# Optimization experiments

Hardware: AMD Instinct MI355X
Metric: run time of the kernel (lower is better)

## Reference

```python
import jax, jax.numpy as jnp
import numpy as np

B, IMG_LEN, TXT_LEN = 32, 49, 77
D, H, HK, FF, NB = 512, 8, 64, 2048, 4
IMG_DIM, VOCAB = 768, 49408
L = IMG_LEN + TXT_LEN

# combined mask: image tokens attend fully; text tokens causal among themselves
_row = np.arange(L)
_KEEP = jnp.asarray(~((_row[:, None] >= IMG_LEN) & (_row[None, :] >= IMG_LEN) & (_row[None, :] > _row[:, None])))  # [L,L] bool


def setup_inputs():
    key = jax.random.key(0)
    ks = jax.random.split(key, 12)
    s = 0.02
    z = lambda *sh: jnp.zeros(sh, jnp.float32)
    o = lambda *sh: jnp.ones(sh, jnp.float32)
    n = lambda k, sh: jax.random.normal(k, sh, jnp.float32) * s
    return {
        'img_hidden': jax.random.normal(ks[0], (B, IMG_LEN, IMG_DIM), jnp.float32),
        'txt_embed': jax.random.normal(ks[1], (B, TXT_LEN, D), jnp.float32),
        'img_proj_w': n(ks[2], (IMG_DIM, D)), 'img_proj_b': z(D),
        'pos_embed': n(ks[3], (L, D)),
        'wq': n(ks[4], (NB, H, D, HK)), 'wk': n(ks[5], (NB, H, D, HK)), 'wv': n(ks[6], (NB, H, D, HK)),
        'w_proj': n(ks[7], (NB, D, D)), 'b_proj': z(NB, D),
        'ln1_g': o(NB, D), 'ln1_b': z(NB, D), 'ln2_g': o(NB, D), 'ln2_b': z(NB, D),
        'fc1_w': n(ks[8], (NB, D, FF)), 'fc1_b': z(NB, FF),
        'fc2_w': n(ks[9], (NB, FF, D)), 'fc2_b': z(NB, D),
        'lnf_g': o(D), 'lnf_b': z(D),
        'out_w': n(ks[10], (D, VOCAB)), 'out_b': z(VOCAB),
        'attention_mask': jnp.ones((B, TXT_LEN), jnp.int32),
    }


def _ln(x, g, b, eps=1e-5):
    mu = x.mean(-1, keepdims=True)
    var = ((x - mu) ** 2).mean(-1, keepdims=True)
    return (x - mu) * jax.lax.rsqrt(var + eps) * g + b


def _forward(img_hidden, txt_embed, img_proj_w, img_proj_b, pos_embed, wq, wk, wv, w_proj, b_proj,
             ln1_g, ln1_b, ln2_g, ln2_b, fc1_w, fc1_b, fc2_w, fc2_b, lnf_g, lnf_b, out_w, out_b,
             attention_mask):
    img = img_hidden @ img_proj_w + img_proj_b + pos_embed[:IMG_LEN]
    txt = txt_embed + pos_embed[IMG_LEN:]
    x = jnp.concatenate([img, txt], axis=1)  # [B,L,D]
    pad = jnp.concatenate([jnp.ones((x.shape[0], IMG_LEN), attention_mask.dtype), attention_mask], axis=1)
    keep = _KEEP[None, None] & (pad[:, None, None, :] != 0)  # [B,1,L,L]
    scale = D ** (-0.5)  # NOTE: original scales by full embed_dim, not head_size (faithful)
    for i in range(NB):
        h = _ln(x, ln1_g[i], ln1_b[i])
        q = jnp.einsum('bld,hdk->bhlk', h, wq[i])
        k = jnp.einsum('bld,hdk->bhlk', h, wk[i])
        v = jnp.einsum('bld,hdk->bhlk', h, wv[i])
        scores = jnp.einsum('bhlk,bhmk->bhlm', q, k) * scale
        scores = jnp.where(keep, scores, -jnp.inf)
        aw = jax.nn.softmax(scores, axis=-1)  # dropout off (eval)
        o = jnp.einsum('bhlm,bhmk->bhlk', aw, v)
        o = o.transpose(0, 2, 1, 3).reshape(x.shape[0], L, H * HK)
        x = x + o @ w_proj[i] + b_proj[i]
        h2 = _ln(x, ln2_g[i], ln2_b[i])
        x = x + jax.nn.gelu(h2 @ fc1_w[i] + fc1_b[i], approximate=False) @ fc2_w[i] + fc2_b[i]
    x = _ln(x, lnf_g, lnf_b)
    return x[:, IMG_LEN:] @ out_w + out_b  # [B,TXT_LEN,VOCAB]


def reference(img_hidden, txt_embed, img_proj_w, img_proj_b, pos_embed, wq, wk, wv, w_proj, b_proj,
              ln1_g, ln1_b, ln2_g, ln2_b, fc1_w, fc1_b, fc2_w, fc2_b, lnf_g, lnf_b, out_w, out_b,
              attention_mask):
    return _forward(img_hidden, txt_embed, img_proj_w, img_proj_b, pos_embed, wq, wk, wv, w_proj, b_proj,
                    ln1_g, ln1_b, ln2_g, ln2_b, fc1_w, fc1_b, fc2_w, fc2_b, lnf_g, lnf_b, out_w, out_b,
                    attention_mask)
```

## Files before the change

### kernel.cpp

```cpp
#include <hip/hip_runtime.h>
#include <hip/hip_bf16.h>
#include <stdint.h>


using u16 = unsigned short;
typedef __attribute__((ext_vector_type(8))) __bf16 bf16x8v;
typedef __attribute__((ext_vector_type(4))) float f32x4;

__device__ __forceinline__ float bf2f(u16 u) {
  union { unsigned int i; float f; } x; x.i = ((unsigned int)u) << 16; return x.f;
}
__device__ __forceinline__ u16 f2bf(float f) {
  union { float f; unsigned int i; } u; u.f = f;
  unsigned int r = u.i + 0x7FFFu + ((u.i >> 16) & 1u);
  return (u16)(r >> 16);
}
__device__ __forceinline__ float ld_f(const void* p, size_t i, int fl) {
  return fl ? ((const float*)p)[i] : bf2f(((const u16*)p)[i]);
}
__device__ __forceinline__ u16 ld_bf(const void* p, size_t i, int fl) {
  return fl ? f2bf(((const float*)p)[i]) : ((const u16*)p)[i];
}

__device__ __forceinline__ void async_copy16(const void* g, void* l) {
  __builtin_amdgcn_global_load_lds(
      (__attribute__((address_space(1))) void*)(g),
      (__attribute__((address_space(3))) void*)(l), 16, 0, 0);
}

__global__ void detect_kernel(const void* __restrict__ img, int* __restrict__ flag) {
  const int lane = threadIdx.x;
  const u16* p = (const u16*)img;
  int bad = 0;
#pragma unroll
  for (int i = 0; i < 4; ++i) {
    float v = bf2f(p[lane * 4 + i]);
    float av = fabsf(v);
    if (!(av <= 1e4f) || (av != 0.0f && av < 1e-30f)) bad++;
  }
#pragma unroll
  for (int off = 32; off; off >>= 1) bad += __shfl_xor(bad, off, 64);
  if (lane == 0) flag[0] = (bad > 16) ? 1 : 0;
}

__global__ void sentinel_kernel(float* out) {
  out[blockIdx.x * 256 + threadIdx.x] = 123456.0f;
}

template <int BM, int BN, int EPI>
__global__ __launch_bounds__(256) void gemm_kernel(
    const u16* __restrict__ A, const u16* __restrict__ Bt, void* Cout,
    const void* __restrict__ bias, long boff, const float* resid,
    const void* __restrict__ pos, int M, int N, int K, int gridM,
    const int* __restrict__ fl)
{
  static_assert(BN == 128, "");
  static_assert(BM == 64 || BM == 128, "");
  constexpr int TILE_B = (BM + BN) * 128;
  constexpr int EPI_B = BM * BN * 2;
  constexpr int SMEM_B = (2 * TILE_B > EPI_B) ? 2 * TILE_B : EPI_B;
  __shared__ __align__(16) char smem[SMEM_B];

  const int tid = threadIdx.x;
  const int lane = tid & 63, wid = tid >> 6;
  const int wm = wid >> 1, wn = wid & 1;
  constexpr int FM = BM / 32, FN = 4;
  constexpr int ITA = BM / 32, ITB = BN / 32;
  constexpr int NLOADS = ITA + ITB;

  const int nwg = gridDim.x;
  const int q = nwg >> 3, r8 = nwg & 7;
  const int xcd = blockIdx.x & 7, idx = blockIdx.x >> 3;
  const int wgid = (xcd < r8 ? xcd * (q + 1) : r8 * (q + 1) + (xcd - r8) * q) + idx;
  const int tileM = (wgid % gridM) * BM, tileN = (wgid / gridM) * BN;

  f32x4 acc[FM][FN] = {};

  auto stage = [&](int buf, int kt) {
    char* base = smem + buf * TILE_B;
#pragma unroll
    for (int it = 0; it < ITA; ++it) {
      int ch = (wid * ITA + it) * 64 + lane;
      int row = ch >> 3, slot = ch & 7;
      int grow = tileM + row; grow = grow < M ? grow : (M - 1);
      async_copy16(A + (size_t)grow * K + kt * 64 + ((slot ^ (row & 7)) << 3),
                   base + (wid * ITA + it) * 1024);
    }
#pragma unroll
    for (int it = 0; it < ITB; ++it) {
      int ch = (wid * ITB + it) * 64 + lane;
      int row = ch >> 3, slot = ch & 7;
      async_copy16(Bt + (size_t)(tileN + row) * K + kt * 64 + ((slot ^ (row & 7)) << 3),
                   base + BM * 128 + (wid * ITB + it) * 1024);
    }
  };

  const int kSteps = K >> 6;
  stage(0, 0);
  int cur = 0;
  for (int kt = 0; kt < kSteps; ++kt) {
    if (kt + 1 < kSteps) {
      stage(cur ^ 1, kt + 1);
      asm volatile("s_waitcnt vmcnt(%0)" :: "i"(NLOADS) : "memory");
    } else {
      asm volatile("s_waitcnt vmcnt(0)" ::: "memory");
    }
    __builtin_amdgcn_s_barrier();
    __builtin_amdgcn_sched_barrier(0);
    const u16* lA = (const u16*)(smem + cur * TILE_B);
    const u16* lB = (const u16*)(smem + cur * TILE_B + BM * 128);
#pragma unroll
    for (int kk = 0; kk < 2; ++kk) {
      const int j = kk * 4 + (lane >> 4);
      bf16x8v af[FM], bfr[FN];
#pragma unroll
      for (int fm = 0; fm < FM; ++fm) {
        int rr = wm * (BM / 2) + fm * 16 + (lane & 15);
        af[fm] = *(const bf16x8v*)(lA + rr * 64 + ((j ^ (rr & 7)) << 3));
      }
#pragma unroll
      for (int fn = 0; fn < FN; ++fn) {
        int rn = wn * 64 + fn * 16 + (lane & 15);
        bfr[fn] = *(const bf16x8v*)(lB + rn * 64 + ((j ^ (rn & 7)) << 3));
      }
      __builtin_amdgcn_s_setprio(1);
#pragma unroll
      for (int fm = 0; fm < FM; ++fm)
#pragma unroll
        for (int fn = 0; fn < FN; ++fn)
          acc[fm][fn] = __builtin_amdgcn_mfma_f32_16x16x32_bf16(
              af[fm], bfr[fn], acc[fm][fn], 0, 0, 0);
      __builtin_amdgcn_s_setprio(0);
    }
    __builtin_amdgcn_sched_barrier(0);
    __builtin_amdgcn_s_barrier();
    cur ^= 1;
  }

  const int fla = (EPI == 0) ? 0 : *fl;
  const int row0l = wm * (BM / 2);
  const int col0l = wn * 64;

  auto store_bf16 = [&](bool do_bias, bool do_gelu) {
    u16* ep = (u16*)smem;
#pragma unroll
    for (int fm = 0; fm < FM; ++fm)
#pragma unroll
      for (int fn = 0; fn < FN; ++fn)
#pragma unroll
        for (int jj = 0; jj < 4; ++jj) {
          int rl = row0l + fm * 16 + ((lane >> 4) << 2) + jj;
          int cl = col0l + fn * 16 + (lane & 15);
          float t = acc[fm][fn][jj];
          if (do_bias) t += ld_f(bias, boff + tileN + cl, fla);
          if (do_gelu) t = 0.5f * t * (1.0f + erff(t * 0.70710678118654752f));
          ep[rl * BN + cl] = f2bf(t);
        }
    __syncthreads();
    for (int rr = tid >> 4; rr < BM; rr += 16) {
      int grow = tileM + rr;
      if (grow < M)
        *(uint4*)((u16*)Cout + (size_t)grow * N + tileN + (tid & 15) * 8) =
            *(const uint4*)(ep + rr * BN + (tid & 15) * 8);
    }
  };

  auto store_f32 = [&](bool do_resid, bool do_remap_pos) {
    float* epf = (float*)smem;
#pragma unroll
    for (int p = 0; p < 2; ++p) {
      __syncthreads();
      if (wm == p) {
#pragma unroll
        for (int fm = 0; fm < FM; ++fm)
#pragma unroll
          for (int fn = 0; fn < FN; ++fn)
#pragma unroll
            for (int jj = 0; jj < 4; ++jj) {
              int rl = fm * 16 + ((lane >> 4) << 2) + jj;
              int cl = col0l + fn * 16 + (lane & 15);
              float t = acc[fm][fn][jj] + ld_f(bias, boff + tileN + cl, fla);
              if (do_remap_pos) {
                int grow_t = tileM + p * (BM / 2) + rl;
                int ll = grow_t % 49;
                t += ld_f(pos, ll * 512 + tileN + cl, fla);
              }
              epf[rl * BN + cl] = t;
            }
      }
      __syncthreads();
      for (int rr = tid >> 5; rr < BM / 2; rr += 8) {
        int grow = tileM + p * (BM / 2) + rr;
        if (grow < M) {
          f32x4 t = *(const f32x4*)(epf + rr * BN + (tid & 31) * 4);
          if (do_resid)
            t += *(const f32x4*)(resid + (size_t)grow * N + tileN + (tid & 31) * 4);
          size_t orow = grow;
          if (do_remap_pos) orow = (size_t)(grow / 49) * 126 + grow % 49;
          *(f32x4*)((float*)Cout + orow * N + tileN + (tid & 31) * 4) = t;
        }
      }
    }
  };

  if constexpr (EPI == 0) store_bf16(false, false);
  else if constexpr (EPI == 1) store_bf16(true, true);
  else if constexpr (EPI == 2) store_f32(true, false);
  else if constexpr (EPI == 3) store_f32(false, true);
  else { if (fla) store_f32(false, false); else store_bf16(true, false); }
}

__global__ __launch_bounds__(512) void gemm256_kernel(
    const u16* __restrict__ A, const u16* __restrict__ Bt, void* Cout,
    const void* __restrict__ bias, int M, int N, int K, int gridM,
    const int* __restrict__ fl)
{
  constexpr int BM = 256, BN = 256;
  constexpr int TILE_B = (BM + BN) * 128;
  __shared__ __align__(16) char smem[2 * TILE_B];

  const int tid = threadIdx.x;
  const int lane = tid & 63, wid = tid >> 6;
  const int wm = wid >> 2, wn = wid & 3;

  const int nwg = gridDim.x;
  const int q = nwg >> 3, r8 = nwg & 7;
  const int xcd = blockIdx.x & 7, idx = blockIdx.x >> 3;
  const int wgid = (xcd < r8 ? xcd * (q + 1) : r8 * (q + 1) + (xcd - r8) * q) + idx;
  const int tileM = (wgid % gridM) * BM, tileN = (wgid / gridM) * BN;

  f32x4 acc[8][4] = {};

  auto stage = [&](int buf, int kt) {
    char* base = smem + buf * TILE_B;
#pragma unroll
    for (int it = 0; it < 4; ++it) {
      int ch = (wid * 4 + it) * 64 + lane;
      int row = ch >> 3, slot = ch & 7;
      int grow = tileM + row; grow = grow < M ? grow : (M - 1);
      async_copy16(A + (size_t)grow * K + kt * 64 + ((slot ^ (row & 7)) << 3),
                   base + (wid * 4 + it) * 1024);
    }
#pragma unroll
    for (int it = 0; it < 4; ++it) {
      int ch = (wid * 4 + it) * 64 + lane;
      int row = ch >> 3, slot = ch & 7;
      async_copy16(Bt + (size_t)(tileN + row) * K + kt * 64 + ((slot ^ (row & 7)) << 3),
                   base + BM * 128 + (wid * 4 + it) * 1024);
    }
  };

  const int kSteps = K >> 6;
  stage(0, 0);
  int cur = 0;
  for (int kt = 0; kt < kSteps; ++kt) {
    if (kt + 1 < kSteps) {
      stage(cur ^ 1, kt + 1);
      asm volatile("s_waitcnt vmcnt(8)" ::: "memory");
    } else {
      asm volatile("s_waitcnt vmcnt(0)" ::: "memory");
    }
    __builtin_amdgcn_s_barrier();
    __builtin_amdgcn_sched_barrier(0);
    const u16* lA = (const u16*)(smem + cur * TILE_B);
    const u16* lB = (const u16*)(smem + cur * TILE_B + BM * 128);
#pragma unroll
    for (int kk = 0; kk < 2; ++kk) {
      const int j = kk * 4 + (lane >> 4);
      bf16x8v bfr[4];
#pragma unroll
      for (int fn = 0; fn < 4; ++fn) {
        int rn = wn * 64 + fn * 16 + (lane & 15);
        bfr[fn] = *(const bf16x8v*)(lB + rn * 64 + ((j ^ (rn & 7)) << 3));
      }
#pragma unroll
      for (int mh = 0; mh < 2; ++mh) {
        bf16x8v af[4];
#pragma unroll
        for (int f = 0; f < 4; ++f) {
          int rr = wm * 128 + (mh * 4 + f) * 16 + (lane & 15);
          af[f] = *(const bf16x8v*)(lA + rr * 64 + ((j ^ (rr & 7)) << 3));
        }
        __builtin_amdgcn_s_setprio(1);
#pragma unroll
        for (int f = 0; f < 4; ++f)
#pragma unroll
          for (int fn = 0; fn < 4; ++fn)
            acc[mh * 4 + f][fn] = __builtin_amdgcn_mfma_f32_16x16x32_bf16(
                af[f], bfr[fn], acc[mh * 4 + f][fn], 0, 0, 0);
        __builtin_amdgcn_s_setprio(0);
      }
    }
    __builtin_amdgcn_sched_barrier(0);
    __builtin_amdgcn_s_barrier();
    cur ^= 1;
  }

  const int fla = *fl;
  if (fla) {
    float* epf = (float*)smem;
#pragma unroll
    for (int p = 0; p < 4; ++p) {
      __syncthreads();
      if (wm == (p >> 1)) {
#pragma unroll
        for (int fq = 0; fq < 4; ++fq) {
          int fm = (p & 1) * 4 + fq;
#pragma unroll
          for (int fn = 0; fn < 4; ++fn)
#pragma unroll
            for (int jj = 0; jj < 4; ++jj) {
              int rl = fq * 16 + ((lane >> 4) << 2) + jj;
              int cl = wn * 64 + fn * 16 + (lane & 15);
              epf[rl * 256 + cl] = acc[fm][fn][jj] + ld_f(bias, tileN + cl, 1);
            }
        }
      }
      __syncthreads();
      for (int rr = tid >> 6; rr < 64; rr += 8) {
        int grow = tileM + p * 64 + rr;
        if (grow < M)
          *(f32x4*)((float*)Cout + (size_t)grow * N + tileN + lane * 4) =
              *(const f32x4*)(epf + rr * 256 + lane * 4);
      }
    }
  } else {
    u16* ep = (u16*)smem;
    __syncthreads();
#pragma unroll
    for (int fm = 0; fm < 8; ++fm)
#pragma unroll
      for (int fn = 0; fn < 4; ++fn)
#pragma unroll
        for (int jj = 0; jj < 4; ++jj) {
          int rl = wm * 128 + fm * 16 + ((lane >> 4) << 2) + jj;
          int cl = wn * 64 + fn * 16 + (lane & 15);
          ep[rl * 256 + cl] = f2bf(acc[fm][fn][jj] + ld_f(bias, tileN + cl, 0));
        }
    __syncthreads();
    for (int rr = tid >> 5; rr < 256; rr += 16) {
      int grow = tileM + rr;
      if (grow < M)
        *(uint4*)((u16*)Cout + (size_t)grow * N + tileN + (tid & 31) * 8) =
            *(const uint4*)(ep + rr * 256 + (tid & 31) * 8);
    }
  }
}

__global__ __launch_bounds__(256) void prep_all(
    const void* __restrict__ imgw, const void* __restrict__ wq,
    const void* __restrict__ wk, const void* __restrict__ wv,
    const void* __restrict__ wp, const void* __restrict__ fc1,
    const void* __restrict__ fc2, const void* __restrict__ imgh,
    const void* __restrict__ txt, const void* __restrict__ pos,
    u16* __restrict__ imgwT, u16* __restrict__ qkvT, u16* __restrict__ wpT,
    u16* __restrict__ fc1T, u16* __restrict__ fc2T,
    u16* __restrict__ imgbf, float* __restrict__ x,
    const int* __restrict__ fl)
{
  const int fla = *fl;
  const int b = blockIdx.x;
  if (b >= 12672) {
    if (b < 17376) {
      int i = (b - 12672) * 256 + threadIdx.x;
      if (i < 1204224) imgbf[i] = ld_bf(imgh, i, fla);
    } else {
      int idx = (b - 17376) * 256 + threadIdx.x;
      if (idx < 32 * 77 * 512) {
        int d = idx & 511, bt = idx >> 9;
        int t = bt % 77, bb = bt / 77;
        x[((size_t)(bb * 126 + 49 + t)) * 512 + d] =
            ld_f(txt, idx, fla) + ld_f(pos, (49 + t) * 512 + d, fla);
      }
    }
    return;
  }
  __shared__ u16 t[32][33];
  const void* in; u16* out; int R, C, cx, ry;
  size_t zi, zo;
  if (b < 384) {
    in = imgw; out = imgwT; R = 768; C = 512; zi = 0; zo = 0;
    cx = b & 15; ry = b >> 4;
  } else if (b < 3456) {
    int bb = b - 384;
    int z = bb >> 5, r2 = bb & 31;
    cx = r2 & 1; ry = r2 >> 1;
    int src = z >> 5, rem = z & 31, li = rem >> 3, hh = rem & 7;
    in = (src == 0) ? wq : (src == 1) ? wk : wv;
    out = qkvT; R = 512; C = 64;
    zi = (size_t)rem * (512 * 64);
    zo = (size_t)li * (1536 * 512) + (size_t)(src * 512 + hh * 64) * 512;
  } else if (b < 4480) {
    int bb = b - 3456;
    int z = bb >> 8, r2 = bb & 255;
    cx = r2 & 15; ry = r2 >> 4;
    in = wp; out = wpT; R = 512; C = 512;
    zi = (size_t)z * (512 * 512); zo = zi;
  } else if (b < 8576) {
    int bb = b - 4480;
    int z = bb >> 10, r2 = bb & 1023;
    cx = r2 & 63; ry = r2 >> 6;
    in = fc1; out = fc1T; R = 512; C = 2048;
    zi = (size_t)z * (512 * 2048); zo = zi;
  } else {
    int bb = b - 8576;
    int z = bb >> 10, r2 = bb & 1023;
    cx = r2 & 15; ry = r2 >> 4;
    in = fc2; out = fc2T; R = 2048; C = 512;
    zi = (size_t)z * (512 * 2048); zo = zi;
  }
  const int c0 = cx * 32, r0 = ry * 32;
  const int tx = threadIdx.x & 31, ty = threadIdx.x >> 5;
#pragma unroll
  for (int i = 0; i < 4; ++i)
    t[ty + 8 * i][tx] = ld_bf(in, zi + (size_t)(r0 + ty + 8 * i) * C + (c0 + tx), fla);
  __syncthreads();
#pragma unroll
  for (int i = 0; i < 4; ++i)
    out[zo + (size_t)(c0 + ty + 8 * i) * R + (r0 + tx)] = t[tx][ty + 8 * i];
}

__global__ __launch_bounds__(256) void transpose_lnf(
    const void* __restrict__ out_w, u16* __restrict__ outwT,
    const float* __restrict__ x, const void* __restrict__ gam,
    const void* __restrict__ bet, u16* __restrict__ xl,
    const int* __restrict__ fl)
{
  const int fla = *fl;
  const int b = blockIdx.x;
  if (b >= 24704) {
    const int lane = threadIdx.x & 63, wid = threadIdx.x >> 6;
    const int r = (b - 24704) * 4 + wid;
    if (r >= 2464) return;
    int bb = r / 77, t = r % 77;
    int srow = bb * 126 + 49 + t;
    const float* xr = x + (size_t)srow * 512 + lane * 8;
    f32x4 v0 = *(const f32x4*)xr;
    f32x4 v1 = *(const f32x4*)(xr + 4);
    float s = v0[0] + v0[1] + v0[2] + v0[3] + v1[0] + v1[1] + v1[2] + v1[3];
#pragma unroll
    for (int off = 32; off; off >>= 1) s += __shfl_xor(s, off, 64);
    const float mu = s * (1.0f / 512.0f);
    float q2 = 0.f;
#pragma unroll
    for (int j = 0; j < 4; ++j) { v0[j] -= mu; q2 += v0[j] * v0[j]; }
#pragma unroll
    for (int j = 0; j < 4; ++j) { v1[j] -= mu; q2 += v1[j] * v1[j]; }
#pragma unroll
    for (int off = 32; off; off >>= 1) q2 += __shfl_xor(q2, off, 64);
    const float inv = rsqrtf(q2 * (1.0f / 512.0f) + 1e-5f);
    union { u16 a[8]; uint4 v; } ou;
#pragma unroll
    for (int j = 0; j < 8; ++j) {
      float d = (j < 4) ? v0[j] : v1[j - 4];
      ou.a[j] = f2bf(d * inv * ld_f(gam, lane * 8 + j, fla)
                     + ld_f(bet, lane * 8 + j, fla));
    }
    *(uint4*)(xl + (size_t)r * 512 + lane * 8) = ou.v;
    return;
  }
  __shared__ u16 t[32][33];
  const int cx = b % 1544, ry = b / 1544;
  const int c0 = cx * 32, r0 = ry * 32;
  const int tx = threadIdx.x & 31, ty = threadIdx.x >> 5;
#pragma unroll
  for (int i = 0; i < 4; ++i)
    t[ty + 8 * i][tx] =
        ld_bf(out_w, (size_t)(r0 + ty + 8 * i) * 49408 + (c0 + tx), fla);
  __syncthreads();
#pragma unroll
  for (int i = 0; i < 4; ++i)
    outwT[(size_t)(c0 + ty + 8 * i) * 512 + (r0 + tx)] = t[tx][ty + 8 * i];
}

__global__ __launch_bounds__(256) void attn_mfma_kernel(
    const u16* __restrict__ qkv, const int* __restrict__ amask,
    u16* __restrict__ o)
{
  const int b = blockIdx.x, hh = blockIdx.y;
  __shared__ __align__(16) u16 Qs[128 * 64];
  __shared__ __align__(16) u16 Ks[128 * 64];
  __shared__ __align__(16) u16 Vt[64 * 136];
  __shared__ float Sf[128 * 129];
  __shared__ __align__(16) u16 Ps[128 * 128];
  __shared__ float padK[128];
  const int tid = threadIdx.x, lane = tid & 63, wid = tid >> 6;

  for (int ch = tid; ch < 1024; ch += 256) {
    int row = ch >> 3, slot = ch & 7;
    int gm = row < 126 ? row : 125;
    size_t base = ((size_t)(b * 126 + gm)) * 1536 + hh * 64;
    int gslot = slot ^ (row & 7);
    *(uint4*)(Qs + row * 64 + slot * 8) = *(const uint4*)(qkv + base + gslot * 8);
    *(uint4*)(Ks + row * 64 + slot * 8) = *(const uint4*)(qkv + base + 512 + gslot * 8);
  }
  for (int m = wid; m < 126; m += 4) {
    size_t base = ((size_t)(b * 126 + m)) * 1536 + hh * 64 + 1024;
    Vt[lane * 136 + m] = qkv[base + lane];
  }
  if (wid == 0) { Vt[lane * 136 + 126] = 0; Vt[lane * 136 + 127] = 0; }
  for (int j = tid; j < 128; j += 256) {
    float kv = 0.0f;
    if (j < 49) kv = 1.0f;
    else if (j < 126) kv = (amask[b * 77 + (j - 49)] != 0) ? 1.0f : 0.0f;
    padK[j] = kv;
  }
  __syncthreads();

  f32x4 accS[2][8] = {};
#pragma unroll
  for (int ks = 0; ks < 2; ++ks) {
    const int j = ks * 4 + (lane >> 4);
    bf16x8v qf[2], kf[8];
#pragma unroll
    for (int fr = 0; fr < 2; ++fr) {
      int rr = (wid * 2 + fr) * 16 + (lane & 15);
      qf[fr] = *(const bf16x8v*)(Qs + rr * 64 + ((j ^ (rr & 7)) << 3));
    }
#pragma unroll
    for (int fc = 0; fc < 8; ++fc) {
      int rn = fc * 16 + (lane & 15);
      kf[fc] = *(const bf16x8v*)(Ks + rn * 64 + ((j ^ (rn & 7)) << 3));
    }
#pragma unroll
    for (int fr = 0; fr < 2; ++fr)
#pragma unroll
      for (int fc = 0; fc < 8; ++fc)
        accS[fr][fc] = __builtin_amdgcn_mfma_f32_16x16x32_bf16(
            qf[fr], kf[fc], accS[fr][fc], 0, 0, 0);
  }
#pragma unroll
  for (int fr = 0; fr < 2; ++fr)
#pragma unroll
    for (int fc = 0; fc < 8; ++fc)
#pragma unroll
      for (int jj = 0; jj < 4; ++jj) {
        int row = (wid * 2 + fr) * 16 + ((lane >> 4) << 2) + jj;
        int col = fc * 16 + (lane & 15);
        Sf[row * 129 + col] = accS[fr][fc][jj];
      }
  __syncthreads();

  const float scale = 0.04419417382415922f;
  for (int r = wid; r < 128; r += 4) {
    const int m0 = lane, m1 = lane + 64;
    float s0 = Sf[r * 129 + m0] * scale;
    float s1 = Sf[r * 129 + m1] * scale;
    bool kp0 = (padK[m0] != 0.f) && (m0 < 49 || r < 49 || m0 <= r);
    bool kp1 = (padK[m1] != 0.f) && (r < 49 || m1 <= r);
    float e0 = kp0 ? s0 : -1e30f;
    float e1 = kp1 ? s1 : -1e30f;
    float mx = fmaxf(e0, e1);
#pragma unroll
    for (int off = 32; off; off >>= 1) mx = fmaxf(mx, __shfl_xor(mx, off, 64));
    float p0 = kp0 ? __expf(s0 - mx) : 0.f;
    float p1 = kp1 ? __expf(s1 - mx) : 0.f;
    float sm = p0 + p1;
#pragma unroll
    for (int off = 32; off; off >>= 1) sm += __shfl_xor(sm, off, 64);
    float inv = 1.0f / sm;
    Ps[r * 128 + (((m0 >> 3) ^ (r & 7)) << 3) + (m0 & 7)] = f2bf(p0 * inv);
    Ps[r * 128 + (((m1 >> 3) ^ (r & 7)) << 3) + (m1 & 7)] = f2bf(p1 * inv);
  }
  __syncthreads();

  f32x4 accO[2][4] = {};
#pragma unroll
  for (int ks = 0; ks < 4; ++ks) {
    const int j = ks * 4 + (lane >> 4);
    bf16x8v pf[2], vf[4];
#pragma unroll
    for (int fr = 0; fr < 2; ++fr) {
      int rr = (wid * 2 + fr) * 16 + (lane & 15);
      pf[fr] = *(const bf16x8v*)(Ps + rr * 128 + ((j ^ (rr & 7)) << 3));
    }
#pragma unroll
    for (int fc = 0; fc < 4; ++fc) {
      int rn = fc * 16 + (lane & 15);
      vf[fc] = *(const bf16x8v*)(Vt + rn * 136 + (j << 3));
    }
#pragma unroll
    for (int fr = 0; fr < 2; ++fr)
#pragma unroll
      for (int fc = 0; fc < 4; ++fc)
        accO[fr][fc] = __builtin_amdgcn_mfma_f32_16x16x32_bf16(
            pf[fr], vf[fc], accO[fr][fc], 0, 0, 0);
  }

  u16* Ol = Qs;
  __syncthreads();
#pragma unroll
  for (int fr = 0; fr < 2; ++fr)
#pragma unroll
    for (int fc = 0; fc < 4; ++fc)
#pragma unroll
      for (int jj = 0; jj < 4; ++jj) {
        int row = (wid * 2 + fr) * 16 + ((lane >> 4) << 2) + jj;
        int col = fc * 16 + (lane & 15);
        Ol[row * 64 + col] = f2bf(accO[fr][fc][jj]);
      }
  __syncthreads();
  for (int r = tid >> 3; r < 126; r += 32) {
    *(uint4*)(o + ((size_t)(b * 126 + r)) * 512 + hh * 64 + (tid & 7) * 8) =
        *(const uint4*)(Ol + r * 64 + (tid & 7) * 8);
  }
}

__global__ __launch_bounds__(256) void ln_kernel(
    const float* __restrict__ x, const void* __restrict__ gam,
    const void* __restrict__ bet, long goff, u16* __restrict__ out,
    int nrows, const int* __restrict__ fl)
{
  const int fla = *fl;
  const int lane = threadIdx.x & 63, wid = threadIdx.x >> 6;
  const int r = blockIdx.x * 4 + wid;
  if (r >= nrows) return;
  const float* xr = x + (size_t)r * 512 + lane * 8;
  f32x4 v0 = *(const f32x4*)xr;
  f32x4 v1 = *(const f32x4*)(xr + 4);
  float s = v0[0] + v0[1] + v0[2] + v0[3] + v1[0] + v1[1] + v1[2] + v1[3];
#pragma unroll
  for (int off = 32; off; off >>= 1) s += __shfl_xor(s, off, 64);
  const float mu = s * (1.0f / 512.0f);
  float q2 = 0.f;
#pragma unroll
  for (int j = 0; j < 4; ++j) { v0[j] -= mu; q2 += v0[j] * v0[j]; }
#pragma unroll
  for (int j = 0; j < 4; ++j) { v1[j] -= mu; q2 += v1[j] * v1[j]; }
#pragma unroll
  for (int off = 32; off; off >>= 1) q2 += __shfl_xor(q2, off, 64);
  const float inv = rsqrtf(q2 * (1.0f / 512.0f) + 1e-5f);
  union { u16 a[8]; uint4 v; } ou;
#pragma unroll
  for (int j = 0; j < 8; ++j) {
    float d = (j < 4) ? v0[j] : v1[j - 4];
    ou.a[j] = f2bf(d * inv * ld_f(gam, goff + lane * 8 + j, fla)
                   + ld_f(bet, goff + lane * 8 + j, fla));
  }
  *(uint4*)(out + (size_t)r * 512 + lane * 8) = ou.v;
}

extern "C" void kernel_launch(void* const* d_in, const int* in_sizes, int n_in,
                              void* d_out, int out_size, void* d_ws, size_t ws_size,
                              hipStream_t stream)
{
  (void)in_sizes; (void)n_in; (void)out_size;
  const void* img_hidden = d_in[0];
  const void* txt_emb    = d_in[1];
  const void* img_proj_w = d_in[2];
  const void* img_proj_b = d_in[3];
  const void* pos_embed  = d_in[4];
  const void* wq    = d_in[5];
  const void* wk    = d_in[6];
  const void* wv    = d_in[7];
  const void* w_proj = d_in[8];
  const void* b_proj = d_in[9];
  const void* ln1_g = d_in[10];
  const void* ln1_b = d_in[11];
  const void* ln2_g = d_in[12];
  const void* ln2_b = d_in[13];
  const void* fc1_w = d_in[14];
  const void* fc1_b = d_in[15];
  const void* fc2_w = d_in[16];
  const void* fc2_b = d_in[17];
  const void* lnf_g = d_in[18];
  const void* lnf_b = d_in[19];
  const void* out_w = d_in[20];
  const void* out_b = d_in[21];
  const int* amask  = (const int*)d_in[22];

  char* ws = (char*)d_ws;
  size_t off = 0;
  auto alloc = [&](size_t bytes) {
    void* p = ws + off; off += (bytes + 255) & ~(size_t)255; return p;
  };
  int* dflag = (int*)alloc(256);
  u16* imgbf = (u16*)alloc(1204224ull * 2);
  float* x   = (float*)alloc(4032ull * 512 * 4);
  u16* xl    = (u16*)alloc(2464ull * 512 * 2);
  const size_t uni0 = off;
  u16* imgwT = (u16*)alloc(512ull * 768 * 2);
  u16* qkvT  = (u16*)alloc(4ull * 1536 * 512 * 2);
  u16* wpT   = (u16*)alloc(4ull * 512 * 512 * 2);
  u16* fc1T  = (u16*)alloc(4ull * 2048 * 512 * 2);
  u16* fc2T  = (u16*)alloc(4ull * 512 * 2048 * 2);
  u16* h     = (u16*)alloc(4032ull * 512 * 2);
  u16* qkvb  = (u16*)alloc(4032ull * 1536 * 2);
  u16* ob    = (u16*)alloc(4032ull * 512 * 2);
  u16* ff    = (u16*)alloc(4032ull * 2048 * 2);
  u16* outwT = (u16*)(ws + uni0);

  if (ws_size < off) {
    sentinel_kernel<<<dim3(16), 256, 0, stream>>>((float*)d_out);
    return;
  }

  detect_kernel<<<dim3(1), 64, 0, stream>>>(img_hidden, dflag);
  prep_all<<<dim3(22304), 256, 0, stream>>>(
      img_proj_w, wq, wk, wv, w_proj, fc1_w, fc2_w, img_hidden, txt_emb,
      pos_embed, imgwT, qkvT, wpT, fc1T, fc2T, imgbf, x, dflag);

  gemm_kernel<64, 128, 3><<<dim3(100), 256, 0, stream>>>(
      imgbf, imgwT, x, img_proj_b, 0, nullptr, pos_embed, 1568, 512, 768, 25, dflag);

  for (int i = 0; i < 4; ++i) {
    ln_kernel<<<dim3(1008), 256, 0, stream>>>(x, ln1_g, ln1_b, i * 512, h, 4032, dflag);
    gemm_kernel<64, 128, 0><<<dim3(756), 256, 0, stream>>>(
        h, qkvT + i * 786432, qkvb, nullptr, 0, nullptr, nullptr, 4032, 1536, 512, 63, dflag);
    attn_mfma_kernel<<<dim3(32, 8), 256, 0, stream>>>(qkvb, amask, ob);
    gemm_kernel<64, 128, 2><<<dim3(252), 256, 0, stream>>>(
        ob, wpT + i * 262144, x, b_proj, i * 512, x, nullptr, 4032, 512, 512, 63, dflag);
    ln_kernel<<<dim3(1008), 256, 0, stream>>>(x, ln2_g, ln2_b, i * 512, h, 4032, dflag);
    gemm_kernel<64, 128, 1><<<dim3(1008), 256, 0, stream>>>(
        h, fc1T + i * 1048576, ff, fc1_b, i * 2048, nullptr, nullptr, 4032, 2048, 512, 63, dflag);
    gemm_kernel<64, 128, 2><<<dim3(252), 256, 0, stream>>>(
        ff, fc2T + i * 1048576, x, fc2_b, i * 512, x, nullptr, 4032, 512, 2048, 63, dflag);
  }

  transpose_lnf<<<dim3(25320), 256, 0, stream>>>(
      out_w, outwT, x, lnf_g, lnf_b, xl, dflag);
  gemm256_kernel<<<dim3(1930), 512, 0, stream>>>(
      xl, outwT, d_out, out_b, 2464, 49408, 512, 10, dflag);
}
```

Baseline: 802.9 us.

## Move out_w transpose into prep, enlarge QKV/FC1 GEMM tiles, prioritize MFMA waves

When the workspace is large enough, the transpose of the vocabulary projection weight moves into the initial prep_all launch, and a standalone final-layernorm kernel replaces the combined transpose+LN kernel at the end. The QKV and FC1 GEMMs switch from 64x128 to 128x128 tiles, halving block count for more reuse per block. The attention kernel raises wave priority around its MFMA loops. Risks include fewer blocks per GPU for the GEMMs and needing an extra workspace region for the transposed output weight.

Result: no change. 803.0 us (median of 2 runs) (+0.0%).

```diff
diff --git a/kernel.cpp b/kernel.cpp
--- a/kernel.cpp
+++ b/kernel.cpp
@@ -353,14 +353,15 @@
     const void* __restrict__ wp, const void* __restrict__ fc1,
     const void* __restrict__ fc2, const void* __restrict__ imgh,
     const void* __restrict__ txt, const void* __restrict__ pos,
+    const void* __restrict__ out_w,
     u16* __restrict__ imgwT, u16* __restrict__ qkvT, u16* __restrict__ wpT,
     u16* __restrict__ fc1T, u16* __restrict__ fc2T,
-    u16* __restrict__ imgbf, float* __restrict__ x,
+    u16* __restrict__ imgbf, float* __restrict__ x, u16* __restrict__ outwT,
     const int* __restrict__ fl)
 {
   const int fla = *fl;
   const int b = blockIdx.x;
-  if (b >= 12672) {
+  if (b >= 12672 && b < 22304) {
     if (b < 17376) {
       int i = (b - 12672) * 256 + threadIdx.x;
       if (i < 1204224) imgbf[i] = ld_bf(imgh, i, fla);
@@ -378,7 +379,11 @@
   __shared__ u16 t[32][33];
   const void* in; u16* out; int R, C, cx, ry;
   size_t zi, zo;
-  if (b < 384) {
+  if (b >= 22304) {
+    int bb = b - 22304;
+    in = out_w; out = outwT; R = 512; C = 49408;
+    cx = bb % 1544; ry = bb / 1544; zi = 0; zo = 0;
+  } else if (b < 384) {
     in = imgw; out = imgwT; R = 768; C = 512; zi = 0; zo = 0;
     cx = b & 15; ry = b >> 4;
   } else if (b < 3456) {
@@ -420,6 +425,42 @@
     out[zo + (size_t)(c0 + ty + 8 * i) * R + (r0 + tx)] = t[tx][ty + 8 * i];
 }
 
+__global__ __launch_bounds__(256) void lnf_kernel(
+    const float* __restrict__ x, const void* __restrict__ gam,
+    const void* __restrict__ bet, u16* __restrict__ xl,
+    const int* __restrict__ fl)
+{
+  const int fla = *fl;
+  const int lane = threadIdx.x & 63, wid = threadIdx.x >> 6;
+  const int r = blockIdx.x * 4 + wid;
+  if (r >= 2464) return;
+  int bb = r / 77, t = r % 77;
+  int srow = bb * 126 + 49 + t;
+  const float* xr = x + (size_t)srow * 512 + lane * 8;
+  f32x4 v0 = *(const f32x4*)xr;
+  f32x4 v1 = *(const f32x4*)(xr + 4);
+  float s = v0[0] + v0[1] + v0[2] + v0[3] + v1[0] + v1[1] + v1[2] + v1[3];
+#pragma unroll
+  for (int off = 32; off; off >>= 1) s += __shfl_xor(s, off, 64);
+  const float mu = s * (1.0f / 512.0f);
+  float q2 = 0.f;
+#pragma unroll
+  for (int j = 0; j < 4; ++j) { v0[j] -= mu; q2 += v0[j] * v0[j]; }
+#pragma unroll
+  for (int j = 0; j < 4; ++j) { v1[j] -= mu; q2 += v1[j] * v1[j]; }
+#pragma unroll
+  for (int off = 32; off; off >>= 1) q2 += __shfl_xor(q2, off, 64);
+  const float inv = rsqrtf(q2 * (1.0f / 512.0f) + 1e-5f);
+  union { u16 a[8]; uint4 v; } ou;
+#pragma unroll
+  for (int j = 0; j < 8; ++j) {
+    float d = (j < 4) ? v0[j] : v1[j - 4];
+    ou.a[j] = f2bf(d * inv * ld_f(gam, lane * 8 + j, fla)
+                   + ld_f(bet, lane * 8 + j, fla));
+  }
+  *(uint4*)(xl + (size_t)r * 512 + lane * 8) = ou.v;
+}
+
 __global__ __launch_bounds__(256) void transpose_lnf(
     const void* __restrict__ out_w, u16* __restrict__ outwT,
     const float* __restrict__ x, const void* __restrict__ gam,
@@ -522,12 +563,14 @@
       int rn = fc * 16 + (lane & 15);
       kf[fc] = *(const bf16x8v*)(Ks + rn * 64 + ((j ^ (rn & 7)) << 3));
     }
+    __builtin_amdgcn_s_setprio(1);
 #pragma unroll
     for (int fr = 0; fr < 2; ++fr)
 #pragma unroll
       for (int fc = 0; fc < 8; ++fc)
         accS[fr][fc] = __builtin_amdgcn_mfma_f32_16x16x32_bf16(
             qf[fr], kf[fc], accS[fr][fc], 0, 0, 0);
+    __builtin_amdgcn_s_setprio(0);
   }
 #pragma unroll
   for (int fr = 0; fr < 2; ++fr)
@@ -579,12 +622,14 @@
       int rn = fc * 16 + (lane & 15);
       vf[fc] = *(const bf16x8v*)(Vt + rn * 136 + (j << 3));
     }
+    __builtin_amdgcn_s_setprio(1);
 #pragma unroll
     for (int fr = 0; fr < 2; ++fr)
 #pragma unroll
       for (int fc = 0; fc < 4; ++fc)
         accO[fr][fc] = __builtin_amdgcn_mfma_f32_16x16x32_bf16(
             pf[fr], vf[fc], accO[fr][fc], 0, 0, 0);
+    __builtin_amdgcn_s_setprio(0);
   }
 
   u16* Ol = Qs;
@@ -688,37 +733,43 @@
   u16* qkvb  = (u16*)alloc(4032ull * 1536 * 2);
   u16* ob    = (u16*)alloc(4032ull * 512 * 2);
   u16* ff    = (u16*)alloc(4032ull * 2048 * 2);
-  u16* outwT = (u16*)(ws + uni0);
 
   if (ws_size < off) {
     sentinel_kernel<<<dim3(16), 256, 0, stream>>>((float*)d_out);
     return;
   }
+  const size_t OUTWT_B = ((49408ull * 512 * 2) + 255) & ~(size_t)255;
+  const bool fuseT = (ws_size >= off + OUTWT_B);
+  u16* outwT = fuseT ? (u16*)(ws + off) : (u16*)(ws + uni0);
 
   detect_kernel<<<dim3(1), 64, 0, stream>>>(img_hidden, dflag);
-  prep_all<<<dim3(22304), 256, 0, stream>>>(
+  prep_all<<<dim3(fuseT ? 47008 : 22304), 256, 0, stream>>>(
       img_proj_w, wq, wk, wv, w_proj, fc1_w, fc2_w, img_hidden, txt_emb,
-      pos_embed, imgwT, qkvT, wpT, fc1T, fc2T, imgbf, x, dflag);
+      pos_embed, out_w, imgwT, qkvT, wpT, fc1T, fc2T, imgbf, x, outwT, dflag);
 
   gemm_kernel<64, 128, 3><<<dim3(100), 256, 0, stream>>>(
       imgbf, imgwT, x, img_proj_b, 0, nullptr, pos_embed, 1568, 512, 768, 25, dflag);
 
   for (int i = 0; i < 4; ++i) {
     ln_kernel<<<dim3(1008), 256, 0, stream>>>(x, ln1_g, ln1_b, i * 512, h, 4032, dflag);
-    gemm_kernel<64, 128, 0><<<dim3(756), 256, 0, stream>>>(
-        h, qkvT + i * 786432, qkvb, nullptr, 0, nullptr, nullptr, 4032, 1536, 512, 63, dflag);
+    gemm_kernel<128, 128, 0><<<dim3(384), 256, 0, stream>>>(
+        h, qkvT + i * 786432, qkvb, nullptr, 0, nullptr, nullptr, 4032, 1536, 512, 32, dflag);
     attn_mfma_kernel<<<dim3(32, 8), 256, 0, stream>>>(qkvb, amask, ob);
     gemm_kernel<64, 128, 2><<<dim3(252), 256, 0, stream>>>(
         ob, wpT + i * 262144, x, b_proj, i * 512, x, nullptr, 4032, 512, 512, 63, dflag);
     ln_kernel<<<dim3(1008), 256, 0, stream>>>(x, ln2_g, ln2_b, i * 512, h, 4032, dflag);
-    gemm_kernel<64, 128, 1><<<dim3(1008), 256, 0, stream>>>(
-        h, fc1T + i * 1048576, ff, fc1_b, i * 2048, nullptr, nullptr, 4032, 2048, 512, 63, dflag);
+    gemm_kernel<128, 128, 1><<<dim3(512), 256, 0, stream>>>(
+        h, fc1T + i * 1048576, ff, fc1_b, i * 2048, nullptr, nullptr, 4032, 2048, 512, 32, dflag);
     gemm_kernel<64, 128, 2><<<dim3(252), 256, 0, stream>>>(
         ff, fc2T + i * 1048576, x, fc2_b, i * 512, x, nullptr, 4032, 512, 2048, 63, dflag);
   }
 
-  transpose_lnf<<<dim3(25320), 256, 0, stream>>>(
-      out_w, outwT, x, lnf_g, lnf_b, xl, dflag);
+  if (fuseT) {
+    lnf_kernel<<<dim3(616), 256, 0, stream>>>(x, lnf_g, lnf_b, xl, dflag);
+  } else {
+    transpose_lnf<<<dim3(25320), 256, 0, stream>>>(
+        out_w, outwT, x, lnf_g, lnf_b, xl, dflag);
+  }
   gemm256_kernel<<<dim3(1930), 512, 0, stream>>>(
       xl, outwT, d_out, out_b, 2464, 49408, 512, 10, dflag);
 }
```
